# Optimization experiments

Measured on AMD Instinct MI355X. Metric: run time of the kernel, lower is better.

## Reference

```python
import jax, jax.numpy as jnp
import numpy as np

PATTERN = np.array([3, 5, 8, 12, 16, 21, 27, 36], dtype=np.int64)
REPEATS = 32
GROUPS = np.tile(PATTERN, REPEATS)   # 256 ragged group sizes
G = int(GROUPS.size)                 # 256 groups
F = int(GROUPS.sum())                # 4096 total features
B = 8192
SPLIT = G - 3                        # split_idx = num_groups - 3
H1, H2 = 512, 256
EPS = 1e-5


def _xavier(key, shape):
    fan_in, fan_out = shape
    lim = float(np.sqrt(6.0 / (fan_in + fan_out)))
    return jax.random.uniform(key, shape, jnp.float32, -lim, lim)


def setup_inputs() -> dict:
    key = jax.random.key(0)
    ks = jax.random.split(key, 8)
    # segment id for every feature column -> its gene group
    seg = jnp.asarray(np.repeat(np.arange(G), GROUPS), dtype=jnp.int32)
    x = jax.random.normal(ks[0], (B, F), jnp.float32)
    # per-group Linear(group,1) weights, flattened; xavier limit per group size
    lims = np.sqrt(6.0 / (GROUPS + 1.0))
    w_gene = jax.random.uniform(ks[1], (F,), jnp.float32, -1.0, 1.0) * jnp.asarray(np.repeat(lims, GROUPS), jnp.float32)
    return {
        "x": x, "seg": seg,
        "w_gene": w_gene, "b_gene": jnp.zeros((G,), jnp.float32),
        "W1g1": _xavier(ks[2], (SPLIT, H1)), "b1g1": jnp.zeros((H1,), jnp.float32),
        "W2g1": _xavier(ks[3], (H1, H2)), "b2g1": jnp.zeros((H2,), jnp.float32),
        "W1g2": _xavier(ks[4], (3, H1)), "b1g2": jnp.zeros((H1,), jnp.float32),
        "W2g2": _xavier(ks[5], (H1, H2)), "b2g2": jnp.zeros((H2,), jnp.float32),
        "gamma1g1": jnp.ones((H1,), jnp.float32), "beta1g1": jnp.zeros((H1,), jnp.float32),
        "gamma2g1": jnp.ones((H2,), jnp.float32), "beta2g1": jnp.zeros((H2,), jnp.float32),
        "gamma1g2": jnp.ones((H1,), jnp.float32), "beta1g2": jnp.zeros((H1,), jnp.float32),
        "gamma2g2": jnp.ones((H2,), jnp.float32), "beta2g2": jnp.zeros((H2,), jnp.float32),
        "W_out": _xavier(ks[6], (2 * H2, 1)), "b_out": jnp.zeros((1,), jnp.float32),
        "W_res": _xavier(ks[7], (G, 1)), "b_res": jnp.zeros((1,), jnp.float32),
    }


def _bn(h, gamma, beta):
    # BatchNorm1d in training mode: biased batch statistics over the batch axis
    mu = jnp.mean(h, axis=0)
    var = jnp.var(h, axis=0)
    return (h - mu) * jax.lax.rsqrt(var + EPS) * gamma + beta


def reference(x, seg, w_gene, b_gene, W1g1, b1g1, W2g1, b2g1, W1g2, b1g2, W2g2, b2g2,
              gamma1g1, beta1g1, gamma2g1, beta2g1, gamma1g2, beta1g2, gamma2g2, beta2g2,
              W_out, b_out, W_res, b_res):
    # The loop of tiny Linear(group,1)+ReLU over contiguous feature slices is
    # exactly a ragged weighted segment-sum: [B, F] -> [B, G]
    gene = jax.nn.relu(jax.ops.segment_sum((x * w_gene).T, seg, num_segments=G).T + b_gene)
    g1, g2 = gene[:, :SPLIT], gene[:, SPLIT:]
    # dropout p = 0.0 -> identity
    h1 = jax.nn.relu(_bn(g1 @ W1g1 + b1g1, gamma1g1, beta1g1))
    h1 = jax.nn.relu(_bn(h1 @ W2g1 + b2g1, gamma2g1, beta2g1))
    h2 = jax.nn.relu(_bn(g2 @ W1g2 + b1g2, gamma1g2, beta1g2))
    h2 = jax.nn.relu(_bn(h2 @ W2g2 + b2g2, gamma2g2, beta2g2))
    combined = jnp.concatenate([h1, h2], axis=1)           # [B, 2*H2]
    return combined @ W_out + b_out + gene @ W_res + b_res  # [B, 1]
```

## Files before the change

kernel.cpp:

```cpp
#include <hip/hip_runtime.h>
#include <cstddef>

#define BATCH  8192
#define NFEAT  4096
#define NGRP   256
#define NSPLIT 253
#define NH1    512
#define NH2    256
#define EPSV   1e-5f

typedef __bf16 bf16_8 __attribute__((ext_vector_type(8)));
typedef float  f32x4  __attribute__((ext_vector_type(4)));

__constant__ int c_prefix[8] = {0,3,8,16,28,44,65,92};
__constant__ int c_gsize[8]  = {3,5,8,12,16,21,27,36};

__global__ __launch_bounds__(256) void gene_aux_kernel(
        const float* __restrict__ x, const float* __restrict__ wg,
        const float* __restrict__ bg, __bf16* __restrict__ geneb,
        const float* __restrict__ W1g1, const float* __restrict__ W2g1,
        const float* __restrict__ W2g2,
        __bf16* __restrict__ w1t, __bf16* __restrict__ w2at, __bf16* __restrict__ w2bt,
        float* __restrict__ st)
{
    __shared__ __align__(16) char smem[(NFEAT + 32 * 8) * 4 + NGRP * 4];
    int t = threadIdx.x;
    int bid = blockIdx.x;

    if (bid >= 8192) {
        int j = bid - 8192;
        if (j == 384) {
            float4 z = {0.f, 0.f, 0.f, 0.f};
#pragma unroll
            for (int i = 0; i < 4; i++) *(float4*)&st[(t + 256 * i) * 4] = z;
            return;
        }
        float (*tile)[33] = (float(*)[33])smem;
        int z = j >> 7, tid = j & 127;
        const float* src; __bf16* dst; int K, N, Kp;
        if (z == 0)      { src = W1g1; dst = w1t;  K = NSPLIT; N = NH1; Kp = 256; }
        else if (z == 1) { src = W2g1; dst = w2at; K = NH1;    N = NH2; Kp = NH1; }
        else             { src = W2g2; dst = w2bt; K = NH1;    N = NH2; Kp = NH1; }
        int ktiles = (K + 31) >> 5;
        if (tid >= ktiles * (N >> 5)) return;
        int kt = (tid % ktiles) * 32, nt = (tid / ktiles) * 32;
        int tx = t & 31, ty = t >> 5;
        for (int r = ty; r < 32; r += 8) {
            int k = kt + r, n = nt + tx;
            tile[r][tx] = (k < K && n < N) ? src[(size_t)k * N + n] : 0.f;
        }
        __syncthreads();
        for (int r = ty; r < 32; r += 8) {
            int n = nt + r, k = kt + tx;
            if (n < N && k < Kp) dst[(size_t)n * Kp + k] = (__bf16)tile[tx][r];
        }
        return;
    }

    float* prod = (float*)smem;
    float* gout = prod + NFEAT + 32 * 8;
    size_t row = bid;
    const float4* xv = (const float4*)(x + row * NFEAT);
    const float4* wv = (const float4*)wg;
#pragma unroll
    for (int i = 0; i < 4; i++) {
        int idx = t + 256 * i;
        float4 a = xv[idx], w = wv[idx];
        float4 p; p.x = a.x*w.x; p.y = a.y*w.y; p.z = a.z*w.z; p.w = a.w*w.w;
        int f = idx * 4;
        *(float4*)&prod[f + ((f >> 7) << 3)] = p;
    }
    __syncthreads();
    int sub = t & 7, gidx = t >> 3;
    int gi  = gidx & 7, fbo = gidx >> 3;
    int pre = c_prefix[gi], len = c_gsize[gi];
#pragma unroll
    for (int s = 0; s < 8; s++) {
        int base = (4 * s + fbo) * 136 + pre;
        float v = 0.f;
        for (int j = sub; j < len; j += 8) v += prod[base + j];
        v += __shfl_down(v, 4, 8);
        v += __shfl_down(v, 2, 8);
        v += __shfl_down(v, 1, 8);
        if (sub == 0) gout[(s << 5) + gidx] = v;
    }
    __syncthreads();
    if (t < 32) {
        unsigned short up[8];
#pragma unroll
        for (int e = 0; e < 8; e++) {
            int g = t * 8 + e;
            __bf16 b = (__bf16)fmaxf(gout[g] + bg[g], 0.f);
            up[e] = *(unsigned short*)&b;
        }
        *(uint4*)((unsigned short*)geneb + row * NGRP + t * 8) = *(uint4*)up;
    }
}

__global__ __launch_bounds__(256) void gemm1_fused(
    const __bf16* __restrict__ geneb, const __bf16* __restrict__ w1t,
    const float* __restrict__ b1g1, __bf16* __restrict__ h1pre,
    float* __restrict__ s1a, float* __restrict__ q1a,
    const float* __restrict__ W1g2, const float* __restrict__ b1g2,
    __bf16* __restrict__ bufA, float* __restrict__ s2a, float* __restrict__ q2a)
{
    __shared__ __align__(16) char smem[19456];
    int t = threadIdx.x;

    if (blockIdx.x == 8) {
        float* Ws  = (float*)smem;
        float* bsh = Ws + 1536;
        float* gv  = bsh + 512;
        for (int i = t; i < 1536; i += 256) Ws[i] = W1g2[i];
        for (int i = t; i < 512; i += 256) bsh[i] = b1g2[i];
        int row0 = blockIdx.y * 64;
        if (t < 192)
            gv[t] = (float)geneb[(size_t)(row0 + t / 3) * NGRP + NSPLIT + (t % 3)];
        __syncthreads();
        int c0 = t, c1 = t + 256;
        float s0 = 0, q0 = 0, s1 = 0, q1 = 0;
        for (int r = 0; r < 64; r++) {
            float a = gv[3 * r], b = gv[3 * r + 1], c = gv[3 * r + 2];
            float v0 = bsh[c0] + a * Ws[c0] + b * Ws[512 + c0] + c * Ws[1024 + c0];
            float v1 = bsh[c1] + a * Ws[c1] + b * Ws[512 + c1] + c * Ws[1024 + c1];
            size_t base = (size_t)(row0 + r) * NH1;
            bufA[base + c0] = (__bf16)v0; bufA[base + c1] = (__bf16)v1;
            s0 += v0; q0 += v0 * v0; s1 += v1; q1 += v1 * v1;
        }
        atomicAdd(&s2a[c0], s0); atomicAdd(&q2a[c0], q0);
        atomicAdd(&s2a[c1], s1); atomicAdd(&q2a[c1], q1);
        return;
    }

    const int K = 256;
    __bf16 (*As)[72] = (__bf16(*)[72])smem;
    __bf16 (*Bs)[72] = (__bf16(*)[72])(smem + 9216);
    float* sred = (float*)(smem + 18432);
    float* qred = sred + 64;

    int n0 = blockIdx.x * 64;
    int m0 = blockIdx.y * 64;
    if (t < 64) { sred[t] = 0.f; qred[t] = 0.f; }

    int lane = t & 63, w = t >> 6;
    int wm = (w & 1) * 32, wn = (w >> 1) * 32;
    int fm = lane & 15, quad = lane >> 4;

    f32x4 acc[2][2];
#pragma unroll
    for (int i = 0; i < 2; i++)
#pragma unroll
        for (int j = 0; j < 2; j++) acc[i][j] = (f32x4){0.f, 0.f, 0.f, 0.f};

    int r0 = t >> 3;
    int kc = (t & 7) * 8;

    for (int kt = 0; kt < (K >> 6); kt++) {
        int kk = kt << 6;
        __syncthreads();
#pragma unroll
        for (int h = 0; h < 2; h++) {
            int row = r0 + h * 32;
            *(uint4*)&As[row][kc] = *(const uint4*)(geneb + (size_t)(m0 + row) * NGRP + kk + kc);
            *(uint4*)&Bs[row][kc] = *(const uint4*)(w1t + (size_t)(n0 + row) * K + kk + kc);
        }
        __syncthreads();
#pragma unroll
        for (int kc2 = 0; kc2 < 64; kc2 += 32) {
            bf16_8 a0 = *(const bf16_8*)&As[wm + fm][kc2 + quad * 8];
            bf16_8 a1 = *(const bf16_8*)&As[wm + 16 + fm][kc2 + quad * 8];
            bf16_8 b0 = *(const bf16_8*)&Bs[wn + fm][kc2 + quad * 8];
            bf16_8 b1 = *(const bf16_8*)&Bs[wn + 16 + fm][kc2 + quad * 8];
            acc[0][0] = __builtin_amdgcn_mfma_f32_16x16x32_bf16(a0, b0, acc[0][0], 0, 0, 0);
            acc[0][1] = __builtin_amdgcn_mfma_f32_16x16x32_bf16(a0, b1, acc[0][1], 0, 0, 0);
            acc[1][0] = __builtin_amdgcn_mfma_f32_16x16x32_bf16(a1, b0, acc[1][0], 0, 0, 0);
            acc[1][1] = __builtin_amdgcn_mfma_f32_16x16x32_bf16(a1, b1, acc[1][1], 0, 0, 0);
        }
    }

    float myS[2] = {0.f, 0.f}, myQ[2] = {0.f, 0.f};
#pragma unroll
    for (int j = 0; j < 2; j++) {
        int col = n0 + wn + j * 16 + fm;
        float bv = b1g1[col];
#pragma unroll
        for (int i = 0; i < 2; i++)
#pragma unroll
            for (int r = 0; r < 4; r++) {
                float v = acc[i][j][r] + bv;
                int row = m0 + wm + i * 16 + quad * 4 + r;
                h1pre[(size_t)row * NH1 + col] = (__bf16)v;
                myS[j] += v; myQ[j] += v * v;
            }
    }
#pragma unroll
    for (int j = 0; j < 2; j++) {
        atomicAdd(&sred[wn + j * 16 + fm], myS[j]);
        atomicAdd(&qred[wn + j * 16 + fm], myQ[j]);
    }
    __syncthreads();
    if (t < 64) {
        atomicAdd(&s1a[n0 + t], sred[t]);
        atomicAdd(&q1a[n0 + t], qred[t]);
    }
}

__global__ __launch_bounds__(256) void gemm2_dual(
    const __bf16* A0, const __bf16* A1,
    const __bf16* WT0, const __bf16* WT1,
    const float* bias0, const float* bias1,
    __bf16* C0, __bf16* C1,
    float* csum0, float* csq0, float* csum1, float* csq1,
    const float* as0, const float* aq0, const float* ag0, const float* ab0,
    const float* as1, const float* aq1, const float* ag1, const float* ab1)
{
    const int K = NH1, n_total = NH2;
    __shared__ __align__(16) __bf16 As[64][72];
    __shared__ __align__(16) __bf16 Bs[64][72];
    __shared__ float bnsc[NH1];
    __shared__ float bnsh[NH1];
    __shared__ float sred[64];
    __shared__ float qred[64];

    int z = blockIdx.z;
    const __bf16* A    = z ? A1 : A0;
    const __bf16* WT   = z ? WT1 : WT0;
    const float*  bias = z ? bias1 : bias0;
    __bf16*       C    = z ? C1 : C0;
    float* csum = z ? csum1 : csum0;
    float* csq  = z ? csq1  : csq0;
    const float* a_sum = z ? as1 : as0;
    const float* a_sq  = z ? aq1 : aq0;
    const float* a_g   = z ? ag1 : ag0;
    const float* a_b   = z ? ab1 : ab0;

    int t = threadIdx.x;
    int n0 = blockIdx.x * 64;
    int m0 = blockIdx.y * 64;
    {
        const float invB = 1.f / (float)BATCH;
        for (int k = t; k < K; k += 256) {
            float mu  = a_sum[k] * invB;
            float var = a_sq[k] * invB - mu * mu;
            float sc  = a_g[k] * rsqrtf(var + EPSV);
            bnsc[k] = sc;
            bnsh[k] = a_b[k] - mu * sc;
        }
    }
    if (t < 64) { sred[t] = 0.f; qred[t] = 0.f; }

    int lane = t & 63, w = t >> 6;
    int wm = (w & 1) * 32, wn = (w >> 1) * 32;
    int fm = lane & 15, quad = lane >> 4;

    f32x4 acc[2][2];
#pragma unroll
    for (int i = 0; i < 2; i++)
#pragma unroll
        for (int j = 0; j < 2; j++) acc[i][j] = (f32x4){0.f, 0.f, 0.f, 0.f};

    int r0 = t >> 3;
    int kc = (t & 7) * 8;

    for (int kt = 0; kt < (K >> 6); kt++) {
        int kk = kt << 6;
        __syncthreads();
#pragma unroll
        for (int h = 0; h < 2; h++) {
            int row = r0 + h * 32;
            uint4 raw = *(const uint4*)(A + (size_t)(m0 + row) * K + kk + kc);
            __bf16 vals[8];
#pragma unroll
            for (int c = 0; c < 4; c++) {
                unsigned uu = (&raw.x)[c];
                int kg = kk + kc + 2 * c;
                float flo = __uint_as_float(uu << 16);
                float fhi = __uint_as_float(uu & 0xffff0000u);
                flo = fmaxf(fmaf(flo, bnsc[kg],     bnsh[kg]),     0.f);
                fhi = fmaxf(fmaf(fhi, bnsc[kg + 1], bnsh[kg + 1]), 0.f);
                vals[2 * c]     = (__bf16)flo;
                vals[2 * c + 1] = (__bf16)fhi;
            }
            *(bf16_8*)&As[row][kc] = *(bf16_8*)vals;
            *(uint4*)&Bs[row][kc] = *(const uint4*)(WT + (size_t)(n0 + row) * K + kk + kc);
        }
        __syncthreads();
#pragma unroll
        for (int kc2 = 0; kc2 < 64; kc2 += 32) {
            bf16_8 a0 = *(const bf16_8*)&As[wm + fm][kc2 + quad * 8];
            bf16_8 a1 = *(const bf16_8*)&As[wm + 16 + fm][kc2 + quad * 8];
            bf16_8 b0 = *(const bf16_8*)&Bs[wn + fm][kc2 + quad * 8];
            bf16_8 b1 = *(const bf16_8*)&Bs[wn + 16 + fm][kc2 + quad * 8];
            acc[0][0] = __builtin_amdgcn_mfma_f32_16x16x32_bf16(a0, b0, acc[0][0], 0, 0, 0);
            acc[0][1] = __builtin_amdgcn_mfma_f32_16x16x32_bf16(a0, b1, acc[0][1], 0, 0, 0);
            acc[1][0] = __builtin_amdgcn_mfma_f32_16x16x32_bf16(a1, b0, acc[1][0], 0, 0, 0);
            acc[1][1] = __builtin_amdgcn_mfma_f32_16x16x32_bf16(a1, b1, acc[1][1], 0, 0, 0);
        }
    }

    float myS[2] = {0.f, 0.f}, myQ[2] = {0.f, 0.f};
#pragma unroll
    for (int j = 0; j < 2; j++) {
        int col = n0 + wn + j * 16 + fm;
        float bv = bias[col];
#pragma unroll
        for (int i = 0; i < 2; i++)
#pragma unroll
            for (int r = 0; r < 4; r++) {
                float v = acc[i][j][r] + bv;
                int row = m0 + wm + i * 16 + quad * 4 + r;
                C[(size_t)row * n_total + col] = (__bf16)v;
                myS[j] += v; myQ[j] += v * v;
            }
    }
#pragma unroll
    for (int j = 0; j < 2; j++) {
        atomicAdd(&sred[wn + j * 16 + fm], myS[j]);
        atomicAdd(&qred[wn + j * 16 + fm], myQ[j]);
    }
    __syncthreads();
    if (t < 64) {
        atomicAdd(&csum[n0 + t], sred[t]);
        atomicAdd(&csq[n0 + t], qred[t]);
    }
}

__global__ __launch_bounds__(256) void final_kernel(
    const __bf16* __restrict__ h1, const __bf16* __restrict__ h2,
    const __bf16* __restrict__ geneb,
    const float* __restrict__ s1, const float* __restrict__ q1,
    const float* __restrict__ gm1, const float* __restrict__ bt1,
    const float* __restrict__ s2, const float* __restrict__ q2,
    const float* __restrict__ gm2, const float* __restrict__ bt2,
    const float* __restrict__ Wout, const float* __restrict__ bo,
    const float* __restrict__ Wres, const float* __restrict__ br,
    float* __restrict__ outp)
{
    int t = threadIdx.x, lane = t & 63, wv = t >> 6;
    int row0 = blockIdx.x * 16 + wv * 4;
    int c = lane * 4;
    const float invB = 1.f / (float)BATCH;
    float4 vs1 = *(const float4*)&s1[c],  vq1 = *(const float4*)&q1[c];
    float4 vg1 = *(const float4*)&gm1[c], vb1 = *(const float4*)&bt1[c];
    float4 vs2 = *(const float4*)&s2[c],  vq2 = *(const float4*)&q2[c];
    float4 vg2 = *(const float4*)&gm2[c], vb2 = *(const float4*)&bt2[c];
    float4 wo1 = *(const float4*)&Wout[c];
    float4 wo2 = *(const float4*)&Wout[NH2 + c];
    float4 wr  = *(const float4*)&Wres[c];
    float4 sc1, sh1, sc2, sh2;
#pragma unroll
    for (int e = 0; e < 4; e++) {
        float mu  = (&vs1.x)[e] * invB;
        float var = (&vq1.x)[e] * invB - mu * mu;
        float sc  = (&vg1.x)[e] * rsqrtf(var + EPSV);
        (&sc1.x)[e] = sc; (&sh1.x)[e] = (&vb1.x)[e] - mu * sc;
        mu  = (&vs2.x)[e] * invB;
        var = (&vq2.x)[e] * invB - mu * mu;
        sc  = (&vg2.x)[e] * rsqrtf(var + EPSV);
        (&sc2.x)[e] = sc; (&sh2.x)[e] = (&vb2.x)[e] - mu * sc;
    }
#pragma unroll
    for (int rr = 0; rr < 4; rr++) {
        int row = row0 + rr;
        ushort4 u1 = *(const ushort4*)((const unsigned short*)h1 + (size_t)row * NH2 + c);
        ushort4 u2 = *(const ushort4*)((const unsigned short*)h2 + (size_t)row * NH2 + c);
        ushort4 ug = *(const ushort4*)((const unsigned short*)geneb + (size_t)row * NGRP + c);
        float acc = 0.f;
#pragma unroll
        for (int e = 0; e < 4; e++) {
            float h1f = __uint_as_float((unsigned)(&u1.x)[e] << 16);
            float h2f = __uint_as_float((unsigned)(&u2.x)[e] << 16);
            float gvf = __uint_as_float((unsigned)(&ug.x)[e] << 16);
            acc += fmaxf(fmaf(h1f, (&sc1.x)[e], (&sh1.x)[e]), 0.f) * (&wo1.x)[e];
            acc += fmaxf(fmaf(h2f, (&sc2.x)[e], (&sh2.x)[e]), 0.f) * (&wo2.x)[e];
            acc += gvf * (&wr.x)[e];
        }
#pragma unroll
        for (int off = 32; off > 0; off >>= 1) acc += __shfl_down(acc, off, 64);
        if (lane == 0) outp[row] = acc + bo[0] + br[0];
    }
}

extern "C" void kernel_launch(void* const* d_in, const int* in_sizes, int n_in,
                              void* d_out, int out_size, void* d_ws, size_t ws_size,
                              hipStream_t stream)
{
    (void)in_sizes; (void)n_in; (void)out_size; (void)ws_size;
    const float* x        = (const float*)d_in[0];
    const float* wgene    = (const float*)d_in[2];
    const float* bgene    = (const float*)d_in[3];
    const float* W1g1     = (const float*)d_in[4];
    const float* b1g1     = (const float*)d_in[5];
    const float* W2g1     = (const float*)d_in[6];
    const float* b2g1     = (const float*)d_in[7];
    const float* W1g2     = (const float*)d_in[8];
    const float* b1g2     = (const float*)d_in[9];
    const float* W2g2     = (const float*)d_in[10];
    const float* b2g2     = (const float*)d_in[11];
    const float* gamma1g1 = (const float*)d_in[12];
    const float* beta1g1  = (const float*)d_in[13];
    const float* gamma2g1 = (const float*)d_in[14];
    const float* beta2g1  = (const float*)d_in[15];
    const float* gamma1g2 = (const float*)d_in[16];
    const float* beta1g2  = (const float*)d_in[17];
    const float* gamma2g2 = (const float*)d_in[18];
    const float* beta2g2  = (const float*)d_in[19];
    const float* Wout     = (const float*)d_in[20];
    const float* bout     = (const float*)d_in[21];
    const float* Wres     = (const float*)d_in[22];
    const float* bres     = (const float*)d_in[23];
    float* outp = (float*)d_out;

    char* p = (char*)d_ws;
    __bf16* geneb = (__bf16*)p;           p += (size_t)BATCH * NGRP * 2;
    __bf16* h1pre = (__bf16*)p;           p += (size_t)BATCH * NH1 * 2;
    __bf16* bufA  = (__bf16*)p;           p += (size_t)BATCH * NH1 * 2;
    __bf16* h1b   = (__bf16*)p;           p += (size_t)BATCH * NH2 * 2;
    __bf16* h2b   = (__bf16*)p;           p += (size_t)BATCH * NH2 * 2;
    __bf16* w1t   = (__bf16*)p;           p += (size_t)NH1 * 256 * 2;
    __bf16* w2at  = (__bf16*)p;           p += (size_t)NH2 * NH1 * 2;
    __bf16* w2bt  = (__bf16*)p;           p += (size_t)NH2 * NH1 * 2;
    float*  st    = (float*)p;
    float* s1a = st;          float* q1a = st + 512;
    float* s1b = st + 1024;   float* q1b = st + 1536;
    float* s2a = st + 2048;   float* q2a = st + 2560;
    float* s2b = st + 3072;   float* q2b = st + 3584;

    gene_aux_kernel<<<8192 + 384 + 1, 256, 0, stream>>>(
        x, wgene, bgene, geneb, W1g1, W2g1, W2g2, w1t, w2at, w2bt, st);

    gemm1_fused<<<dim3(9, BATCH / 64), 256, 0, stream>>>(
        geneb, w1t, b1g1, h1pre, s1a, q1a,
        W1g2, b1g2, bufA, s2a, q2a);

    gemm2_dual<<<dim3(NH2 / 64, BATCH / 64, 2), 256, 0, stream>>>(
        h1pre, bufA, w2at, w2bt, b2g1, b2g2, h1b, h2b,
        s1b, q1b, s2b, q2b,
        s1a, q1a, gamma1g1, beta1g1,
        s2a, q2a, gamma1g2, beta1g2);

    final_kernel<<<BATCH / 16, 256, 0, stream>>>(
        h1b, h2b, geneb,
        s1b, q1b, gamma2g1, beta2g1,
        s2b, q2b, gamma2g2, beta2g2,
        Wout, bout, Wres, bres, outp);
}
```

Baseline: 274.9 us.

## Load GEMM B fragments directly from global and remap blocks across XCDs

Both GEMM kernels stop staging the weight (B) tile in shared memory. Each lane instead reads its bf16x8 MFMA fragment straight from global memory, which relies on the small weight matrices staying cache-resident. This cuts LDS footprint and store traffic and may let more blocks fit per CU, at the cost of repeated uncoalesced global loads. The grid is also flattened and remapped so consecutive block IDs (round-robined across the 8 XCDs) share row tiles, aiming at better L2 locality for the A operand.

```diff
diff --git a/kernel.cpp b/kernel.cpp
--- a/kernel.cpp
+++ b/kernel.cpp
@@ -104,16 +104,22 @@
     const float* __restrict__ W1g2, const float* __restrict__ b1g2,
     __bf16* __restrict__ bufA, float* __restrict__ s2a, float* __restrict__ q2a)
 {
-    __shared__ __align__(16) char smem[19456];
+    __shared__ __align__(16) char smem[9984];
     int t = threadIdx.x;
 
-    if (blockIdx.x == 8) {
+    int L = blockIdx.x;
+    int g = L & 7, cc = L >> 3;
+    int yq = cc / 9;
+    int bx = cc - 9 * yq;
+    int by = g + 8 * yq;
+
+    if (bx == 8) {
         float* Ws  = (float*)smem;
         float* bsh = Ws + 1536;
         float* gv  = bsh + 512;
         for (int i = t; i < 1536; i += 256) Ws[i] = W1g2[i];
         for (int i = t; i < 512; i += 256) bsh[i] = b1g2[i];
-        int row0 = blockIdx.y * 64;
+        int row0 = by * 64;
         if (t < 192)
             gv[t] = (float)geneb[(size_t)(row0 + t / 3) * NGRP + NSPLIT + (t % 3)];
         __syncthreads();
@@ -134,12 +140,11 @@
 
     const int K = 256;
     __bf16 (*As)[72] = (__bf16(*)[72])smem;
-    __bf16 (*Bs)[72] = (__bf16(*)[72])(smem + 9216);
-    float* sred = (float*)(smem + 18432);
+    float* sred = (float*)(smem + 9216);
     float* qred = sred + 64;
 
-    int n0 = blockIdx.x * 64;
-    int m0 = blockIdx.y * 64;
+    int n0 = bx * 64;
+    int m0 = by * 64;
     if (t < 64) { sred[t] = 0.f; qred[t] = 0.f; }
 
     int lane = t & 63, w = t >> 6;
@@ -154,6 +159,8 @@
 
     int r0 = t >> 3;
     int kc = (t & 7) * 8;
+    const __bf16* Brow0 = w1t + (size_t)(n0 + wn + fm) * K;
+    const __bf16* Brow1 = w1t + (size_t)(n0 + wn + 16 + fm) * K;
 
     for (int kt = 0; kt < (K >> 6); kt++) {
         int kk = kt << 6;
@@ -162,15 +169,14 @@
         for (int h = 0; h < 2; h++) {
             int row = r0 + h * 32;
             *(uint4*)&As[row][kc] = *(const uint4*)(geneb + (size_t)(m0 + row) * NGRP + kk + kc);
-            *(uint4*)&Bs[row][kc] = *(const uint4*)(w1t + (size_t)(n0 + row) * K + kk + kc);
         }
         __syncthreads();
 #pragma unroll
         for (int kc2 = 0; kc2 < 64; kc2 += 32) {
             bf16_8 a0 = *(const bf16_8*)&As[wm + fm][kc2 + quad * 8];
             bf16_8 a1 = *(const bf16_8*)&As[wm + 16 + fm][kc2 + quad * 8];
-            bf16_8 b0 = *(const bf16_8*)&Bs[wn + fm][kc2 + quad * 8];
-            bf16_8 b1 = *(const bf16_8*)&Bs[wn + 16 + fm][kc2 + quad * 8];
+            bf16_8 b0 = *(const bf16_8*)&Brow0[kk + kc2 + quad * 8];
+            bf16_8 b1 = *(const bf16_8*)&Brow1[kk + kc2 + quad * 8];
             acc[0][0] = __builtin_amdgcn_mfma_f32_16x16x32_bf16(a0, b0, acc[0][0], 0, 0, 0);
             acc[0][1] = __builtin_amdgcn_mfma_f32_16x16x32_bf16(a0, b1, acc[0][1], 0, 0, 0);
             acc[1][0] = __builtin_amdgcn_mfma_f32_16x16x32_bf16(a1, b0, acc[1][0], 0, 0, 0);
@@ -216,7 +222,6 @@
 {
     const int K = NH1, n_total = NH2;
     __shared__ __align__(16) __bf16 As[64][72];
-    __shared__ __align__(16) __bf16 Bs[64][72];
     __shared__ float bnsc[NH1];
     __shared__ float bnsh[NH1];
     __shared__ float sred[64];
@@ -234,9 +239,15 @@
     const float* a_g   = z ? ag1 : ag0;
     const float* a_b   = z ? ab1 : ab0;
 
+    int L = blockIdx.x;
+    int g = L & 7, cc = L >> 3;
+    int yq = cc >> 2;
+    int bx = cc & 3;
+    int by = g + 8 * yq;
+
     int t = threadIdx.x;
-    int n0 = blockIdx.x * 64;
-    int m0 = blockIdx.y * 64;
+    int n0 = bx * 64;
+    int m0 = by * 64;
     {
         const float invB = 1.f / (float)BATCH;
         for (int k = t; k < K; k += 256) {
@@ -261,6 +272,8 @@
 
     int r0 = t >> 3;
     int kc = (t & 7) * 8;
+    const __bf16* Brow0 = WT + (size_t)(n0 + wn + fm) * K;
+    const __bf16* Brow1 = WT + (size_t)(n0 + wn + 16 + fm) * K;
 
     for (int kt = 0; kt < (K >> 6); kt++) {
         int kk = kt << 6;
@@ -282,15 +295,14 @@
                 vals[2 * c + 1] = (__bf16)fhi;
             }
             *(bf16_8*)&As[row][kc] = *(bf16_8*)vals;
-            *(uint4*)&Bs[row][kc] = *(const uint4*)(WT + (size_t)(n0 + row) * K + kk + kc);
         }
         __syncthreads();
 #pragma unroll
         for (int kc2 = 0; kc2 < 64; kc2 += 32) {
             bf16_8 a0 = *(const bf16_8*)&As[wm + fm][kc2 + quad * 8];
             bf16_8 a1 = *(const bf16_8*)&As[wm + 16 + fm][kc2 + quad * 8];
-            bf16_8 b0 = *(const bf16_8*)&Bs[wn + fm][kc2 + quad * 8];
-            bf16_8 b1 = *(const bf16_8*)&Bs[wn + 16 + fm][kc2 + quad * 8];
+            bf16_8 b0 = *(const bf16_8*)&Brow0[kk + kc2 + quad * 8];
+            bf16_8 b1 = *(const bf16_8*)&Brow1[kk + kc2 + quad * 8];
             acc[0][0] = __builtin_amdgcn_mfma_f32_16x16x32_bf16(a0, b0, acc[0][0], 0, 0, 0);
             acc[0][1] = __builtin_amdgcn_mfma_f32_16x16x32_bf16(a0, b1, acc[0][1], 0, 0, 0);
             acc[1][0] = __builtin_amdgcn_mfma_f32_16x16x32_bf16(a1, b0, acc[1][0], 0, 0, 0);
@@ -429,11 +441,11 @@
     gene_aux_kernel<<<8192 + 384 + 1, 256, 0, stream>>>(
         x, wgene, bgene, geneb, W1g1, W2g1, W2g2, w1t, w2at, w2bt, st);
 
-    gemm1_fused<<<dim3(9, BATCH / 64), 256, 0, stream>>>(
+    gemm1_fused<<<9 * (BATCH / 64), 256, 0, stream>>>(
         geneb, w1t, b1g1, h1pre, s1a, q1a,
         W1g2, b1g2, bufA, s2a, q2a);
 
-    gemm2_dual<<<dim3(NH2 / 64, BATCH / 64, 2), 256, 0, stream>>>(
+    gemm2_dual<<<dim3((NH2 / 64) * (BATCH / 64), 1, 2), 256, 0, stream>>>(
         h1pre, bufA, w2at, w2bt, b2g1, b2g2, h1b, h2b,
         s1b, q1b, s2b, q2b,
         s1a, q1a, gamma1g1, beta1g1,
```

New measurement: 280.3 us. Within noise of the previous version (+2.0%).
